# Kernel optimization log

Hardware: AMD Instinct MI355X
Metric: run time of the kernel (lower is better)

Reference implementation:

```python
import jax, jax.numpy as jnp
import numpy as np

D = 1024
K = 3  # depthwise conv kernel size, causal (left pad K-1)


def setup_inputs() -> dict:
    key = jax.random.key(0)
    ks = jax.random.split(key, 6)
    B, L = 16, 2048
    x = jax.random.normal(ks[0], (B, L, D), dtype=jnp.float32)
    s_in = 1.0 / np.sqrt(D)
    Win = jax.random.uniform(ks[1], (3 * D, D), minval=-s_in, maxval=s_in, dtype=jnp.float32)
    bin_ = jax.random.uniform(ks[2], (3 * D,), minval=-s_in, maxval=s_in, dtype=jnp.float32)
    # depthwise Conv1d weight (D, 1, K) -> stored as (D, K)
    s_c = 1.0 / np.sqrt(K)  # fan_in = in_channels/groups * K = K
    wconv = jax.random.uniform(ks[3], (D, K), minval=-s_c, maxval=s_c, dtype=jnp.float32)
    Wout = jax.random.uniform(ks[4], (D, D), minval=-s_in, maxval=s_in, dtype=jnp.float32)
    bout = jax.random.uniform(ks[5], (D,), minval=-s_in, maxval=s_in, dtype=jnp.float32)
    return {"x": x, "Win": Win, "bin_": bin_, "wconv": wconv, "Wout": Wout, "bout": bout}


def reference(x, Win, bin_, wconv, Wout, bout):
    # x: (B, L, D). in_proj -> (B, L, 3D); chunk along channel dim == last dim here
    BCx = jnp.einsum('bld,ed->ble', x, Win) + bin_
    Bg, Cg, xg = jnp.split(BCx, 3, axis=-1)  # each (B, L, D)
    Bx = Bg * xg
    L = Bx.shape[1]
    # causal depthwise conv: pad K-1 zeros on the left of time axis
    xp = jnp.pad(Bx, ((0, 0), (K - 1, 0), (0, 0)))
    conv_out = (wconv[:, 0] * xp[:, 0:L]
                + wconv[:, 1] * xp[:, 1:L + 1]
                + wconv[:, 2] * xp[:, 2:L + 2])  # (B, L, D)
    y = Cg * conv_out
    return jnp.einsum('bld,ed->ble', y, Wout) + bout
```

## Files before the change

kernel.cpp:

```cpp
#include <hip/hip_runtime.h>
#include <hip/hip_bf16.h>

#define D_    1024
#define LSEQ  2048
#define M_    32768
#define K_    1024
#define BK    32

typedef __bf16 bf16x8 __attribute__((ext_vector_type(8)));
typedef float  f32x4  __attribute__((ext_vector_type(4)));

__device__ __forceinline__ unsigned short f2bf(float f) {
  unsigned u = __float_as_uint(f);
  u += 0x7FFFu + ((u >> 16) & 1u);
  return (unsigned short)(u >> 16);
}
__device__ __forceinline__ float bf2f(unsigned short h) {
  return __uint_as_float(((unsigned)h) << 16);
}

__device__ __forceinline__ void gload_lds16(const void* g, void* l) {
  __builtin_amdgcn_global_load_lds((const __attribute__((address_space(1))) void*)g,
                                   (__attribute__((address_space(3))) void*)l,
                                   16, 0, 0);
}

#define NX4  (M_ * K_ / 4)
#define NW4  (3072 * K_ / 4)
#define NO4  (D_ * K_ / 4)
__global__ __launch_bounds__(256) void cvt_all(const float* __restrict__ x,
                                               const float* __restrict__ Win,
                                               const float* __restrict__ Wout,
                                               unsigned short* __restrict__ x_b,
                                               unsigned short* __restrict__ Win_b,
                                               unsigned short* __restrict__ Wout_b) {
  int i = blockIdx.x * 256 + threadIdx.x;
  const float* src;
  unsigned short* dst;
  int off;
  if (i < NX4)            { src = x;    dst = x_b;    off = i; }
  else if (i < NX4 + NW4) { src = Win;  dst = Win_b;  off = i - NX4; }
  else                    { src = Wout; dst = Wout_b; off = i - NX4 - NW4; }
  float4 v = ((const float4*)src)[off];
  ushort4 o;
  o.x = f2bf(v.x); o.y = f2bf(v.y); o.z = f2bf(v.z); o.w = f2bf(v.w);
  ((ushort4*)dst)[off] = o;
}

__global__ __launch_bounds__(256) void gemm_inproj(const unsigned short* __restrict__ A,
                                                   const unsigned short* __restrict__ Wb,
                                                   const float* __restrict__ bin,
                                                   unsigned short* __restrict__ Bx,
                                                   unsigned short* __restrict__ Cg) {
  __shared__ __align__(16) char smem[16896];
  unsigned short* As = (unsigned short*)smem;
  unsigned short* Bs = (unsigned short*)(smem + 8192);
  float* tr = (float*)smem;

  const int g   = blockIdx.x;
  const int xcd = g & 7;
  const int u   = g >> 3;
  const int m0  = (xcd + 8 * (u / 24)) * 128;
  const int c   = u % 24;
  const int paired = (c < 16);

  const int tid  = threadIdx.x;
  const int lane = tid & 63;
  const int wave = tid >> 6;
  const int quad = lane >> 4;
  const int l16  = lane & 15;
  const int wm   = wave & 1;
  const int wn   = wave >> 1;

  int n0;
  const unsigned short* B0p;
  const unsigned short* B1p;
  if (paired) {
    n0  = c * 64;
    B0p = Wb + (long)n0 * K_;
    B1p = Wb + (long)(2048 + n0) * K_;
  } else {
    n0  = (c - 16) * 128;
    B0p = Wb + (long)(1024 + n0) * K_;
    B1p = B0p + (long)64 * K_;
  }

  const int r0 = tid >> 2;
  const int s0 = (tid & 3) * 8;
  const unsigned short* a0 = A + (long)(m0 + r0) * K_ + s0;
  const unsigned short* a1 = a0 + (long)64 * K_;
  const unsigned short* b0 = B0p + (long)r0 * K_ + s0;
  const unsigned short* b1 = B1p + (long)r0 * K_ + s0;
  unsigned short* lA0 = &As[tid * 8];
  unsigned short* lA1 = &As[(256 + tid) * 8];
  unsigned short* lB0 = &Bs[tid * 8];
  unsigned short* lB1 = &Bs[(256 + tid) * 8];

  f32x4 acc[4][4] = {};

  for (int k0 = 0; k0 < K_; k0 += BK) {
    gload_lds16(a0 + k0, lA0);
    gload_lds16(a1 + k0, lA1);
    gload_lds16(b0 + k0, lB0);
    gload_lds16(b1 + k0, lB1);
    __syncthreads();

    bf16x8 af[4], bfr[4];
#pragma unroll
    for (int mi = 0; mi < 4; ++mi)
      af[mi] = *(const bf16x8*)&As[(wm * 64 + mi * 16 + l16) * BK + quad * 8];
#pragma unroll
    for (int ni = 0; ni < 4; ++ni)
      bfr[ni] = *(const bf16x8*)&Bs[(wn * 64 + ni * 16 + l16) * BK + quad * 8];

#pragma unroll
    for (int mi = 0; mi < 4; ++mi)
#pragma unroll
      for (int ni = 0; ni < 4; ++ni)
        acc[mi][ni] = __builtin_amdgcn_mfma_f32_16x16x32_bf16(af[mi], bfr[ni],
                                                              acc[mi][ni], 0, 0, 0);
    __syncthreads();
  }

  float bv[4];
#pragma unroll
  for (int ni = 0; ni < 4; ++ni) {
    int col = wn * 64 + ni * 16 + l16;
    if (paired)
      bv[ni] = (col < 64) ? bin[n0 + col] : bin[2048 + n0 + col - 64];
    else
      bv[ni] = bin[1024 + n0 + col];
  }

  const int rr   = tid >> 3;
  const int cgid = tid & 7;

#pragma unroll
  for (int mi = 0; mi < 4; ++mi) {
#pragma unroll
    for (int ni = 0; ni < 4; ++ni) {
      int col = wn * 64 + ni * 16 + l16;
      f32x4 v = acc[mi][ni];
#pragma unroll
      for (int r = 0; r < 4; ++r)
        tr[(wm * 16 + quad * 4 + r) * 132 + col] = v[r] + bv[ni];
    }
    __syncthreads();

    int grow = m0 + (rr >> 4) * 64 + mi * 16 + (rr & 15);

    if (paired) {
#pragma unroll
      for (int j = 0; j < 2; ++j) {
        int cc = (cgid + j * 8) * 4;
        f32x4 bg = *(const f32x4*)&tr[rr * 132 + cc];
        f32x4 xg = *(const f32x4*)&tr[rr * 132 + 64 + cc];
        ushort4 o;
        o.x = f2bf(bg[0] * xg[0]); o.y = f2bf(bg[1] * xg[1]);
        o.z = f2bf(bg[2] * xg[2]); o.w = f2bf(bg[3] * xg[3]);
        *(ushort4*)&Bx[(long)grow * D_ + n0 + cc] = o;
      }
    } else {
#pragma unroll
      for (int j = 0; j < 4; ++j) {
        int cc = (cgid + j * 8) * 4;
        f32x4 v = *(const f32x4*)&tr[rr * 132 + cc];
        ushort4 o;
        o.x = f2bf(v[0]); o.y = f2bf(v[1]); o.z = f2bf(v[2]); o.w = f2bf(v[3]);
        *(ushort4*)&Cg[(long)grow * D_ + n0 + cc] = o;
      }
    }
    __syncthreads();
  }
}

__global__ __launch_bounds__(256) void conv_mul(const unsigned short* __restrict__ Bx,
                                                const unsigned short* __restrict__ Cg,
                                                const float* __restrict__ wconv,
                                                unsigned short* __restrict__ y) {
  __shared__ float wt[3][D_];
  for (int i = threadIdx.x; i < D_; i += 256) {
    wt[0][i] = wconv[i * 3 + 0];
    wt[1][i] = wconv[i * 3 + 1];
    wt[2][i] = wconv[i * 3 + 2];
  }
  __syncthreads();

  int idx = blockIdx.x * 256 + threadIdx.x;
  int bl  = idx >> 7;
  int d8  = (idx & 127) * 8;
  int l   = bl & (LSEQ - 1);

  typedef unsigned short us8 __attribute__((ext_vector_type(8)));
  us8 zz = {0, 0, 0, 0, 0, 0, 0, 0};
  us8 x0 = *(const us8*)&Bx[(long)bl * D_ + d8];
  us8 x1 = (l >= 1) ? *(const us8*)&Bx[(long)(bl - 1) * D_ + d8] : zz;
  us8 x2 = (l >= 2) ? *(const us8*)&Bx[(long)(bl - 2) * D_ + d8] : zz;
  us8 cg = *(const us8*)&Cg[(long)bl * D_ + d8];

  us8 o;
#pragma unroll
  for (int j = 0; j < 8; ++j) {
    float conv = wt[0][d8 + j] * bf2f(x2[j]) + wt[1][d8 + j] * bf2f(x1[j])
               + wt[2][d8 + j] * bf2f(x0[j]);
    o[j] = f2bf(bf2f(cg[j]) * conv);
  }
  *(us8*)&y[(long)bl * D_ + d8] = o;
}

__global__ __launch_bounds__(256) void gemm_out(const unsigned short* __restrict__ A,
                                                const unsigned short* __restrict__ Wb,
                                                const float* __restrict__ bias,
                                                float* __restrict__ Out) {
  __shared__ __align__(16) char smem[16896];
  unsigned short* As = (unsigned short*)smem;
  unsigned short* Bs = (unsigned short*)(smem + 8192);
  float* tr = (float*)smem;

  const int g   = blockIdx.x;
  const int u   = g >> 3;
  const int m0  = ((g & 7) + 8 * (u >> 3)) * 128;
  const int n0  = (u & 7) * 128;

  const int tid  = threadIdx.x;
  const int lane = tid & 63;
  const int wave = tid >> 6;
  const int quad = lane >> 4;
  const int l16  = lane & 15;
  const int wm   = wave & 1;
  const int wn   = wave >> 1;

  const int r0 = tid >> 2;
  const int s0 = (tid & 3) * 8;
  const unsigned short* a0 = A + (long)(m0 + r0) * K_ + s0;
  const unsigned short* a1 = a0 + (long)64 * K_;
  const unsigned short* b0 = Wb + (long)(n0 + r0) * K_ + s0;
  const unsigned short* b1 = b0 + (long)64 * K_;
  unsigned short* lA0 = &As[tid * 8];
  unsigned short* lA1 = &As[(256 + tid) * 8];
  unsigned short* lB0 = &Bs[tid * 8];
  unsigned short* lB1 = &Bs[(256 + tid) * 8];

  f32x4 acc[4][4] = {};

  for (int k0 = 0; k0 < K_; k0 += BK) {
    gload_lds16(a0 + k0, lA0);
    gload_lds16(a1 + k0, lA1);
    gload_lds16(b0 + k0, lB0);
    gload_lds16(b1 + k0, lB1);
    __syncthreads();

    bf16x8 af[4], bfr[4];
#pragma unroll
    for (int mi = 0; mi < 4; ++mi)
      af[mi] = *(const bf16x8*)&As[(wm * 64 + mi * 16 + l16) * BK + quad * 8];
#pragma unroll
    for (int ni = 0; ni < 4; ++ni)
      bfr[ni] = *(const bf16x8*)&Bs[(wn * 64 + ni * 16 + l16) * BK + quad * 8];

#pragma unroll
    for (int mi = 0; mi < 4; ++mi)
#pragma unroll
      for (int ni = 0; ni < 4; ++ni)
        acc[mi][ni] = __builtin_amdgcn_mfma_f32_16x16x32_bf16(af[mi], bfr[ni],
                                                              acc[mi][ni], 0, 0, 0);
    __syncthreads();
  }

  float bv[4];
#pragma unroll
  for (int ni = 0; ni < 4; ++ni)
    bv[ni] = bias[n0 + wn * 64 + ni * 16 + l16];

  const int rr   = tid >> 3;
  const int cgid = tid & 7;

#pragma unroll
  for (int mi = 0; mi < 4; ++mi) {
#pragma unroll
    for (int ni = 0; ni < 4; ++ni) {
      int col = wn * 64 + ni * 16 + l16;
      f32x4 v = acc[mi][ni];
#pragma unroll
      for (int r = 0; r < 4; ++r)
        tr[(wm * 16 + quad * 4 + r) * 132 + col] = v[r] + bv[ni];
    }
    __syncthreads();

    int grow = m0 + (rr >> 4) * 64 + mi * 16 + (rr & 15);
#pragma unroll
    for (int j = 0; j < 4; ++j) {
      int cc = (cgid + j * 8) * 4;
      f32x4 v = *(const f32x4*)&tr[rr * 132 + cc];
      *(f32x4*)&Out[(long)grow * D_ + n0 + cc] = v;
    }
    __syncthreads();
  }
}

extern "C" void kernel_launch(void* const* d_in, const int* in_sizes, int n_in,
                              void* d_out, int out_size, void* d_ws, size_t ws_size,
                              hipStream_t stream) {
  const float* x     = (const float*)d_in[0];
  const float* Win   = (const float*)d_in[1];
  const float* bin   = (const float*)d_in[2];
  const float* wconv = (const float*)d_in[3];
  const float* Wout  = (const float*)d_in[4];
  const float* bout  = (const float*)d_in[5];

  char* ws = (char*)d_ws;
  unsigned short* x_b    = (unsigned short*)(ws);
  unsigned short* Win_b  = (unsigned short*)(ws + 67108864);
  unsigned short* Wout_b = (unsigned short*)(ws + 73400320);
  unsigned short* Bx_b   = (unsigned short*)(ws + 75497472);
  unsigned short* Cg_b   = (unsigned short*)(ws + 142606336);
  unsigned short* y_b    = (unsigned short*)(ws + 209715200);

  cvt_all<<<(NX4 + NW4 + NO4) / 256, 256, 0, stream>>>(x, Win, Wout, x_b, Win_b, Wout_b);

  gemm_inproj<<<6144, 256, 0, stream>>>(x_b, Win_b, bin, Bx_b, Cg_b);

  conv_mul<<<(M_ * (D_ / 8)) / 256, 256, 0, stream>>>(Bx_b, Cg_b, wconv, y_b);

  gemm_out<<<2048, 256, 0, stream>>>(y_b, Wout_b, bout, (float*)d_out);
}
```

Baseline: 601.2 us.

## Rewrite GEMMs with 256x256 tiles, double-buffered LDS, swizzling and 8-wave schedule

Both GEMM kernels now share a core that computes 256x256 output tiles per 512-thread block with BK=64, double-buffered 128KB LDS staging via global_load_lds, and an XOR swizzle to avoid bank conflicts. The inner loop interleaves LDS fragment loads and MFMA quarters with barriers and s_setprio to overlap memory and math across waves. The goal is higher arithmetic intensity and latency hiding than the small 128x128 single-buffered tiles. The tradeoff is much larger LDS use and register pressure (8x4 accumulators), which limits occupancy and risks spills.

```diff
diff --git a/kernel.cpp b/kernel.cpp
--- a/kernel.cpp
+++ b/kernel.cpp
@@ -5,7 +5,7 @@
 #define LSEQ  2048
 #define M_    32768
 #define K_    1024
-#define BK    32
+#define NT    16
 
 typedef __bf16 bf16x8 __attribute__((ext_vector_type(8)));
 typedef float  f32x4  __attribute__((ext_vector_type(4)));
@@ -24,6 +24,9 @@
                                    (__attribute__((address_space(3))) void*)l,
                                    16, 0, 0);
 }
+
+#define FENCE() asm volatile("" ::: "memory")
+#define RBAR()  do { FENCE(); __builtin_amdgcn_s_barrier(); FENCE(); } while (0)
 
 #define NX4  (M_ * K_ / 4)
 #define NW4  (3072 * K_ / 4)
@@ -47,114 +50,169 @@
   ((ushort4*)dst)[off] = o;
 }
 
-__global__ __launch_bounds__(256) void gemm_inproj(const unsigned short* __restrict__ A,
-                                                   const unsigned short* __restrict__ Wb,
-                                                   const float* __restrict__ bin,
-                                                   unsigned short* __restrict__ Bx,
-                                                   unsigned short* __restrict__ Cg) {
-  __shared__ __align__(16) char smem[16896];
-  unsigned short* As = (unsigned short*)smem;
-  unsigned short* Bs = (unsigned short*)(smem + 8192);
-  float* tr = (float*)smem;
-
-  const int g   = blockIdx.x;
-  const int xcd = g & 7;
-  const int u   = g >> 3;
-  const int m0  = (xcd + 8 * (u / 24)) * 128;
-  const int c   = u % 24;
-  const int paired = (c < 16);
-
+
+#define LDA(mh) do { _Pragma("unroll") \
+  for (int f = 0; f < 4; ++f) { \
+    const int o = aRow + ((mh) * 4 + f) * 2048; \
+    av[f][0] = *(const bf16x8*)(As + o); \
+    av[f][1] = *(const bf16x8*)(As + (o ^ 64)); \
+  } } while (0)
+
+#define LDB(nh, bb) do { _Pragma("unroll") \
+  for (int f = 0; f < 2; ++f) { \
+    const int o = bRow + ((nh) * 2 + f) * 2048; \
+    bb[f][0] = *(const bf16x8*)(Bs + o); \
+    bb[f][1] = *(const bf16x8*)(Bs + (o ^ 64)); \
+  } } while (0)
+
+#define MFMA_Q(mh, nh, bb) do { _Pragma("unroll") \
+  for (int f = 0; f < 4; ++f) { _Pragma("unroll") \
+    for (int gg = 0; gg < 2; ++gg) { \
+      f32x4 cacc = acc[(mh) * 4 + f][(nh) * 2 + gg]; \
+      cacc = __builtin_amdgcn_mfma_f32_16x16x32_bf16(av[f][0], bb[gg][0], cacc, 0, 0, 0); \
+      cacc = __builtin_amdgcn_mfma_f32_16x16x32_bf16(av[f][1], bb[gg][1], cacc, 0, 0, 0); \
+      acc[(mh) * 4 + f][(nh) * 2 + gg] = cacc; \
+    } } } while (0)
+
+__device__ __forceinline__ void gemm_core256(char* smem,
+    const unsigned short* aBase,
+    const unsigned short* b0p, const unsigned short* b1p,
+    const unsigned short* b2p, const unsigned short* b3p,
+    f32x4 acc[8][4]) {
   const int tid  = threadIdx.x;
   const int lane = tid & 63;
-  const int wave = tid >> 6;
+  const int wm   = (tid >> 6) >> 2;
+  const int wn   = (tid >> 6) & 3;
   const int quad = lane >> 4;
   const int l16  = lane & 15;
-  const int wm   = wave & 1;
-  const int wn   = wave >> 1;
-
+  const int swz  = (quad ^ (l16 & 7)) << 4;
+  const int aRow = ((wm << 7) + l16) * 128 + swz;
+  const int bRow = ((wn << 6) + l16) * 128 + swz;
+
+  auto STAGE = [&](int t) {
+    char* lb = smem + ((t & 1) << 16);
+    const int k0 = t << 6;
+#pragma unroll
+    for (int i = 0; i < 4; ++i)
+      gload_lds16(aBase + ((long)i << 16) + k0, lb + tid * 16 + i * 8192);
+    gload_lds16(b0p + k0, lb + 32768 + tid * 16);
+    gload_lds16(b1p + k0, lb + 32768 + tid * 16 + 8192);
+    gload_lds16(b2p + k0, lb + 32768 + tid * 16 + 16384);
+    gload_lds16(b3p + k0, lb + 32768 + tid * 16 + 24576);
+  };
+
+  STAGE(0);
+  STAGE(1);
+  asm volatile("s_waitcnt vmcnt(8)" ::: "memory");
+  RBAR();
+
+  for (int t = 0; t < NT; ++t) {
+    const char* As = smem + ((t & 1) << 16);
+    const char* Bs = As + 32768;
+    bf16x8 av[4][2], b0[2][2], b1[2][2];
+
+    LDA(0); LDB(0, b0);
+    RBAR();
+    __builtin_amdgcn_s_setprio(1); MFMA_Q(0, 0, b0); __builtin_amdgcn_s_setprio(0);
+    RBAR();
+    LDB(1, b1);
+    RBAR();
+    __builtin_amdgcn_s_setprio(1); MFMA_Q(0, 1, b1); __builtin_amdgcn_s_setprio(0);
+    RBAR();
+    LDA(1);
+    RBAR();
+    __builtin_amdgcn_s_setprio(1); MFMA_Q(1, 1, b1); __builtin_amdgcn_s_setprio(0);
+    RBAR();
+    LDB(0, b0);
+    RBAR();
+    __builtin_amdgcn_s_setprio(1); MFMA_Q(1, 0, b0); __builtin_amdgcn_s_setprio(0);
+    RBAR();
+
+    if (t + 2 < NT) {
+      STAGE(t + 2);
+      asm volatile("s_waitcnt vmcnt(8)" ::: "memory");
+      RBAR();
+    } else if (t + 2 == NT) {
+      asm volatile("s_waitcnt vmcnt(0)" ::: "memory");
+      RBAR();
+    }
+  }
+}
+
+__global__ __launch_bounds__(512, 2) void gemm_inproj(const unsigned short* __restrict__ A,
+                                                      const unsigned short* __restrict__ Wb,
+                                                      const float* __restrict__ bin,
+                                                      unsigned short* __restrict__ Bx,
+                                                      unsigned short* __restrict__ Cg) {
+  __shared__ __align__(16) char smem[131072];
+
+  const int g  = blockIdx.x;
+  const int u  = g >> 3;
+  const int m0 = ((g & 7) + 8 * (u / 12)) * 256;
+  const int c  = u % 12;
+  const bool paired = (c < 8);
+
+  const int tid  = threadIdx.x;
+  const int lane = tid & 63;
+  const int srow = ((tid >> 6) << 3) + (lane >> 3);
+  const int sch  = (lane & 7) ^ (lane >> 3);
+
+  const unsigned short* aBase = A + (long)(m0 + srow) * K_ + sch * 8;
+  const unsigned short *b0p, *b1p, *b2p, *b3p;
   int n0;
-  const unsigned short* B0p;
-  const unsigned short* B1p;
   if (paired) {
-    n0  = c * 64;
-    B0p = Wb + (long)n0 * K_;
-    B1p = Wb + (long)(2048 + n0) * K_;
+    n0  = c * 128;
+    b0p = Wb + (long)(n0 + srow) * K_ + sch * 8;
+    b1p = b0p + (long)64 * K_;
+    b2p = Wb + (long)(2048 + n0 + srow) * K_ + sch * 8;
+    b3p = b2p + (long)64 * K_;
   } else {
-    n0  = (c - 16) * 128;
-    B0p = Wb + (long)(1024 + n0) * K_;
-    B1p = B0p + (long)64 * K_;
-  }
-
-  const int r0 = tid >> 2;
-  const int s0 = (tid & 3) * 8;
-  const unsigned short* a0 = A + (long)(m0 + r0) * K_ + s0;
-  const unsigned short* a1 = a0 + (long)64 * K_;
-  const unsigned short* b0 = B0p + (long)r0 * K_ + s0;
-  const unsigned short* b1 = B1p + (long)r0 * K_ + s0;
-  unsigned short* lA0 = &As[tid * 8];
-  unsigned short* lA1 = &As[(256 + tid) * 8];
-  unsigned short* lB0 = &Bs[tid * 8];
-  unsigned short* lB1 = &Bs[(256 + tid) * 8];
-
-  f32x4 acc[4][4] = {};
-
-  for (int k0 = 0; k0 < K_; k0 += BK) {
-    gload_lds16(a0 + k0, lA0);
-    gload_lds16(a1 + k0, lA1);
-    gload_lds16(b0 + k0, lB0);
-    gload_lds16(b1 + k0, lB1);
-    __syncthreads();
-
-    bf16x8 af[4], bfr[4];
-#pragma unroll
-    for (int mi = 0; mi < 4; ++mi)
-      af[mi] = *(const bf16x8*)&As[(wm * 64 + mi * 16 + l16) * BK + quad * 8];
-#pragma unroll
-    for (int ni = 0; ni < 4; ++ni)
-      bfr[ni] = *(const bf16x8*)&Bs[(wn * 64 + ni * 16 + l16) * BK + quad * 8];
-
-#pragma unroll
-    for (int mi = 0; mi < 4; ++mi)
-#pragma unroll
-      for (int ni = 0; ni < 4; ++ni)
-        acc[mi][ni] = __builtin_amdgcn_mfma_f32_16x16x32_bf16(af[mi], bfr[ni],
-                                                              acc[mi][ni], 0, 0, 0);
-    __syncthreads();
-  }
-
-  float bv[4];
+    n0  = (c - 8) * 256;
+    b0p = Wb + (long)(1024 + n0 + srow) * K_ + sch * 8;
+    b1p = b0p + (long)64 * K_;
+    b2p = b0p + (long)128 * K_;
+    b3p = b0p + (long)192 * K_;
+  }
+
+  f32x4 acc[8][4] = {};
+  gemm_core256(smem, aBase, b0p, b1p, b2p, b3p, acc);
+
+  const int wm = (tid >> 6) >> 2, wn = (tid >> 6) & 3;
+  const int quad = lane >> 4, l16 = lane & 15;
+  float* tr = (float*)smem;
+
+  float bvv[4];
 #pragma unroll
   for (int ni = 0; ni < 4; ++ni) {
     int col = wn * 64 + ni * 16 + l16;
-    if (paired)
-      bv[ni] = (col < 64) ? bin[n0 + col] : bin[2048 + n0 + col - 64];
-    else
-      bv[ni] = bin[1024 + n0 + col];
-  }
-
-  const int rr   = tid >> 3;
-  const int cgid = tid & 7;
-
-#pragma unroll
-  for (int mi = 0; mi < 4; ++mi) {
+    bvv[ni] = paired ? ((col < 128) ? bin[n0 + col] : bin[2048 + n0 + col - 128])
+                     : bin[1024 + n0 + col];
+  }
+
+  const int trr   = tid >> 4;
+  const int tcc   = tid & 15;
+  const int growb = m0 + ((trr >> 4) << 7) + (trr & 15);
+
+#pragma unroll
+  for (int mi = 0; mi < 8; ++mi) {
+    __syncthreads();
 #pragma unroll
     for (int ni = 0; ni < 4; ++ni) {
       int col = wn * 64 + ni * 16 + l16;
       f32x4 v = acc[mi][ni];
 #pragma unroll
       for (int r = 0; r < 4; ++r)
-        tr[(wm * 16 + quad * 4 + r) * 132 + col] = v[r] + bv[ni];
+        tr[(wm * 16 + quad * 4 + r) * 260 + col] = v[r] + bvv[ni];
     }
     __syncthreads();
 
-    int grow = m0 + (rr >> 4) * 64 + mi * 16 + (rr & 15);
-
+    const int grow = growb + mi * 16;
     if (paired) {
 #pragma unroll
       for (int j = 0; j < 2; ++j) {
-        int cc = (cgid + j * 8) * 4;
-        f32x4 bg = *(const f32x4*)&tr[rr * 132 + cc];
-        f32x4 xg = *(const f32x4*)&tr[rr * 132 + 64 + cc];
+        int cc = tcc * 4 + j * 64;
+        f32x4 bg = *(const f32x4*)&tr[trr * 260 + cc];
+        f32x4 xg = *(const f32x4*)&tr[trr * 260 + 128 + cc];
         ushort4 o;
         o.x = f2bf(bg[0] * xg[0]); o.y = f2bf(bg[1] * xg[1]);
         o.z = f2bf(bg[2] * xg[2]); o.w = f2bf(bg[3] * xg[3]);
@@ -163,14 +221,13 @@
     } else {
 #pragma unroll
       for (int j = 0; j < 4; ++j) {
-        int cc = (cgid + j * 8) * 4;
-        f32x4 v = *(const f32x4*)&tr[rr * 132 + cc];
+        int cc = tcc * 4 + j * 64;
+        f32x4 v = *(const f32x4*)&tr[trr * 260 + cc];
         ushort4 o;
         o.x = f2bf(v[0]); o.y = f2bf(v[1]); o.z = f2bf(v[2]); o.w = f2bf(v[3]);
         *(ushort4*)&Cg[(long)grow * D_ + n0 + cc] = o;
       }
     }
-    __syncthreads();
   }
 }
 
@@ -208,93 +265,61 @@
   *(us8*)&y[(long)bl * D_ + d8] = o;
 }
 
-__global__ __launch_bounds__(256) void gemm_out(const unsigned short* __restrict__ A,
-                                                const unsigned short* __restrict__ Wb,
-                                                const float* __restrict__ bias,
-                                                float* __restrict__ Out) {
-  __shared__ __align__(16) char smem[16896];
-  unsigned short* As = (unsigned short*)smem;
-  unsigned short* Bs = (unsigned short*)(smem + 8192);
-  float* tr = (float*)smem;
-
-  const int g   = blockIdx.x;
-  const int u   = g >> 3;
-  const int m0  = ((g & 7) + 8 * (u >> 3)) * 128;
-  const int n0  = (u & 7) * 128;
+__global__ __launch_bounds__(512, 2) void gemm_out(const unsigned short* __restrict__ A,
+                                                   const unsigned short* __restrict__ Wb,
+                                                   const float* __restrict__ bias,
+                                                   float* __restrict__ Out) {
+  __shared__ __align__(16) char smem[131072];
+
+  const int g  = blockIdx.x;
+  const int u  = g >> 3;
+  const int m0 = ((g & 7) + 8 * (u >> 2)) * 256;
+  const int n0 = (u & 3) * 256;
 
   const int tid  = threadIdx.x;
   const int lane = tid & 63;
-  const int wave = tid >> 6;
-  const int quad = lane >> 4;
-  const int l16  = lane & 15;
-  const int wm   = wave & 1;
-  const int wn   = wave >> 1;
-
-  const int r0 = tid >> 2;
-  const int s0 = (tid & 3) * 8;
-  const unsigned short* a0 = A + (long)(m0 + r0) * K_ + s0;
-  const unsigned short* a1 = a0 + (long)64 * K_;
-  const unsigned short* b0 = Wb + (long)(n0 + r0) * K_ + s0;
-  const unsigned short* b1 = b0 + (long)64 * K_;
-  unsigned short* lA0 = &As[tid * 8];
-  unsigned short* lA1 = &As[(256 + tid) * 8];
-  unsigned short* lB0 = &Bs[tid * 8];
-  unsigned short* lB1 = &Bs[(256 + tid) * 8];
-
-  f32x4 acc[4][4] = {};
-
-  for (int k0 = 0; k0 < K_; k0 += BK) {
-    gload_lds16(a0 + k0, lA0);
-    gload_lds16(a1 + k0, lA1);
-    gload_lds16(b0 + k0, lB0);
-    gload_lds16(b1 + k0, lB1);
+  const int srow = ((tid >> 6) << 3) + (lane >> 3);
+  const int sch  = (lane & 7) ^ (lane >> 3);
+
+  const unsigned short* aBase = A + (long)(m0 + srow) * K_ + sch * 8;
+  const unsigned short* b0p   = Wb + (long)(n0 + srow) * K_ + sch * 8;
+
+  f32x4 acc[8][4] = {};
+  gemm_core256(smem, aBase, b0p, b0p + (long)64 * K_, b0p + (long)128 * K_,
+               b0p + (long)192 * K_, acc);
+
+  const int wm = (tid >> 6) >> 2, wn = (tid >> 6) & 3;
+  const int quad = lane >> 4, l16 = lane & 15;
+  float* tr = (float*)smem;
+
+  float bvv[4];
+#pragma unroll
+  for (int ni = 0; ni < 4; ++ni)
+    bvv[ni] = bias[n0 + wn * 64 + ni * 16 + l16];
+
+  const int trr   = tid >> 4;
+  const int tcc   = tid & 15;
+  const int growb = m0 + ((trr >> 4) << 7) + (trr & 15);
+
+#pragma unroll
+  for (int mi = 0; mi < 8; ++mi) {
     __syncthreads();
-
-    bf16x8 af[4], bfr[4];
-#pragma unroll
-    for (int mi = 0; mi < 4; ++mi)
-      af[mi] = *(const bf16x8*)&As[(wm * 64 + mi * 16 + l16) * BK + quad * 8];
-#pragma unroll
-    for (int ni = 0; ni < 4; ++ni)
-      bfr[ni] = *(const bf16x8*)&Bs[(wn * 64 + ni * 16 + l16) * BK + quad * 8];
-
-#pragma unroll
-    for (int mi = 0; mi < 4; ++mi)
-#pragma unroll
-      for (int ni = 0; ni < 4; ++ni)
-        acc[mi][ni] = __builtin_amdgcn_mfma_f32_16x16x32_bf16(af[mi], bfr[ni],
-                                                              acc[mi][ni], 0, 0, 0);
-    __syncthreads();
-  }
-
-  float bv[4];
-#pragma unroll
-  for (int ni = 0; ni < 4; ++ni)
-    bv[ni] = bias[n0 + wn * 64 + ni * 16 + l16];
-
-  const int rr   = tid >> 3;
-  const int cgid = tid & 7;
-
-#pragma unroll
-  for (int mi = 0; mi < 4; ++mi) {
 #pragma unroll
     for (int ni = 0; ni < 4; ++ni) {
       int col = wn * 64 + ni * 16 + l16;
       f32x4 v = acc[mi][ni];
 #pragma unroll
       for (int r = 0; r < 4; ++r)
-        tr[(wm * 16 + quad * 4 + r) * 132 + col] = v[r] + bv[ni];
+        tr[(wm * 16 + quad * 4 + r) * 260 + col] = v[r] + bvv[ni];
     }
     __syncthreads();
 
-    int grow = m0 + (rr >> 4) * 64 + mi * 16 + (rr & 15);
+    const int grow = growb + mi * 16;
 #pragma unroll
     for (int j = 0; j < 4; ++j) {
-      int cc = (cgid + j * 8) * 4;
-      f32x4 v = *(const f32x4*)&tr[rr * 132 + cc];
-      *(f32x4*)&Out[(long)grow * D_ + n0 + cc] = v;
-    }
-    __syncthreads();
+      int cc = tcc * 4 + j * 64;
+      *(f32x4*)&Out[(long)grow * D_ + n0 + cc] = *(const f32x4*)&tr[trr * 260 + cc];
+    }
   }
 }
 
@@ -318,9 +343,9 @@
 
   cvt_all<<<(NX4 + NW4 + NO4) / 256, 256, 0, stream>>>(x, Win, Wout, x_b, Win_b, Wout_b);
 
-  gemm_inproj<<<6144, 256, 0, stream>>>(x_b, Win_b, bin, Bx_b, Cg_b);
+  gemm_inproj<<<1536, 512, 0, stream>>>(x_b, Win_b, bin, Bx_b, Cg_b);
 
   conv_mul<<<(M_ * (D_ / 8)) / 256, 256, 0, stream>>>(Bx_b, Cg_b, wconv, y_b);
 
-  gemm_out<<<2048, 256, 0, stream>>>(y_b, Wout_b, bout, (float*)d_out);
-}
+  gemm_out<<<512, 512, 0, stream>>>(y_b, Wout_b, bout, (float*)d_out);
+}
```

After: 567.0 us. 5.7% less time.
